# Kernel optimization log

Hardware: AMD Instinct MI355X
Metric: run time of the kernel (lower is better)

## Reference

```python
import jax, jax.numpy as jnp
import numpy as np

N, D_IN, H, D_EMB = 2048, 128, 256, 64


def setup_inputs() -> dict:
    key = jax.random.key(0)
    ks = jax.random.split(key, 8)
    x = jax.random.normal(ks[0], (N, D_IN), dtype=jnp.float32)
    adj = jnp.zeros((N, N), dtype=jnp.float32)  # only its last dim is used (eye sizing)
    s = 0.05
    W0 = jax.random.normal(ks[1], (D_IN, H), dtype=jnp.float32) * s
    b0 = jnp.zeros((H,), dtype=jnp.float32)
    W1 = jax.random.normal(ks[2], (H, D_EMB), dtype=jnp.float32) * s
    b1 = jnp.zeros((D_EMB,), dtype=jnp.float32)
    W2 = jax.random.normal(ks[3], (D_IN, D_IN), dtype=jnp.float32) * s
    b2 = jnp.zeros((D_IN,), dtype=jnp.float32)
    temp = jnp.float32(0.1)
    theta = jnp.float32(0.1)
    return {"x": x, "adj": adj, "W0": W0, "b0": b0, "W1": W1, "b1": b1,
            "W2": W2, "b2": b2, "temp": temp, "theta": theta}


def reference(x, adj, W0, b0, W1, b1, W2, b2, temp, theta):
    # layer 0 (on x) and middle layer 1 (on out_x), both with ReLU activation
    out_x = jax.nn.relu(x @ W0 + b0)            # [N, H]
    emb = jax.nn.relu(out_x @ W1 + b1)          # [N, D_EMB]
    # last layer is applied to the ORIGINAL x (per the `x = model(x)` branch)
    x_last = x @ W2 + b2                        # [N, D_IN]

    # dist[i,j] = -||emb_i - emb_j||^2, computed via the gemm expansion
    sq = jnp.sum(emb * emb, axis=1)             # [N]
    dist = -(sq[:, None] + sq[None, :] - 2.0 * (emb @ emb.T))  # [N, N]

    prob = jax.nn.sigmoid((1.0 + temp) * dist + (5.0 + theta))
    A = prob + jnp.eye(adj.shape[-1], dtype=prob.dtype)        # [N, N]

    # diag(A.sum(-1))^{-1} @ A @ x_last  ==  rowwise divide by degree
    deg = jnp.sum(A, axis=-1)                   # [N]
    out = jax.nn.relu((A @ x_last) / deg[:, None])

    # sigmoid(.) > 0 everywhere, so all N*N entries are nonzero: adj_wts is the
    # full flattened adjacency (data-independent shape, jit-safe)
    adj_wts = A.reshape(-1)
    return out, adj_wts
```

## Files before the change

kernel.cpp:

```cpp
#include <hip/hip_runtime.h>
#include <hip/hip_bf16.h>


typedef short bf16x8 __attribute__((ext_vector_type(8)));
typedef float f32x4 __attribute__((ext_vector_type(4)));

__device__ __forceinline__ unsigned short f2bf(float f) {
    unsigned u = __float_as_uint(f);
    unsigned r = u + 0x7fffu + ((u >> 16) & 1u);
    return (unsigned short)(r >> 16);
}

__global__ __launch_bounds__(512) void k1_mlp(
    const float* __restrict__ x,
    const float* __restrict__ W0, const float* __restrict__ b0,
    const float* __restrict__ W1, const float* __restrict__ b1,
    const float* __restrict__ W2, const float* __restrict__ b2,
    unsigned short* __restrict__ emb_bf,
    unsigned short* __restrict__ xlT_bf,
    float* __restrict__ sq)
{
    __shared__ float xs[8 * 132];
    __shared__ float oxs[8 * 260];
    __shared__ unsigned short xls[128 * 8];
    const int t = threadIdx.x;
    const int r0 = blockIdx.x * 8;

    if (t < 256) {
        int row = t >> 5, c4 = t & 31;
        float4 v = *(const float4*)(x + (r0 + row) * 128 + c4 * 4);
        *(float4*)(&xs[row * 132 + c4 * 4]) = v;
    }
    __syncthreads();

    {
        int c = t & 255, rg = t >> 8;
        float bb = b0[c];
        float acc[4] = {bb, bb, bb, bb};
        for (int kk = 0; kk < 32; ++kk) {
            float wa = W0[(kk * 4 + 0) * 256 + c];
            float wb = W0[(kk * 4 + 1) * 256 + c];
            float wc = W0[(kk * 4 + 2) * 256 + c];
            float wd = W0[(kk * 4 + 3) * 256 + c];
            #pragma unroll
            for (int r = 0; r < 4; ++r) {
                float4 xv = *(const float4*)(&xs[(rg * 4 + r) * 132 + kk * 4]);
                acc[r] += xv.x * wa + xv.y * wb + xv.z * wc + xv.w * wd;
            }
        }
        #pragma unroll
        for (int r = 0; r < 4; ++r) oxs[(rg * 4 + r) * 260 + c] = fmaxf(acc[r], 0.0f);
    }
    __syncthreads();

    {
        int h = t & 63, r = t >> 6;
        float acc = b1[h];
        for (int kk = 0; kk < 64; ++kk) {
            float wa = W1[(kk * 4 + 0) * 64 + h];
            float wb = W1[(kk * 4 + 1) * 64 + h];
            float wc = W1[(kk * 4 + 2) * 64 + h];
            float wd = W1[(kk * 4 + 3) * 64 + h];
            float4 xv = *(const float4*)(&oxs[r * 260 + kk * 4]);
            acc += xv.x * wa + xv.y * wb + xv.z * wc + xv.w * wd;
        }
        float e = fmaxf(acc, 0.0f);
        emb_bf[(r0 + r) * 64 + h] = f2bf(e);
        float s = e * e;
        #pragma unroll
        for (int off = 32; off; off >>= 1) s += __shfl_xor(s, off);
        if (h == 0) sq[r0 + r] = s;
    }

    {
        int c = t & 127, rg = t >> 7;
        float bb = b2[c];
        float acc[2] = {bb, bb};
        for (int kk = 0; kk < 32; ++kk) {
            float wa = W2[(kk * 4 + 0) * 128 + c];
            float wb = W2[(kk * 4 + 1) * 128 + c];
            float wc = W2[(kk * 4 + 2) * 128 + c];
            float wd = W2[(kk * 4 + 3) * 128 + c];
            #pragma unroll
            for (int r = 0; r < 2; ++r) {
                float4 xv = *(const float4*)(&xs[(rg * 2 + r) * 132 + kk * 4]);
                acc[r] += xv.x * wa + xv.y * wb + xv.z * wc + xv.w * wd;
            }
        }
        unsigned short p0 = f2bf(acc[0]), p1 = f2bf(acc[1]);
        *(unsigned int*)(&xls[c * 8 + rg * 2]) = (unsigned)p0 | ((unsigned)p1 << 16);
    }
    __syncthreads();
    if (t < 128) {
        uint4 v = *(const uint4*)(&xls[t * 8]);
        *(uint4*)(&xlT_bf[t * 2048 + r0]) = v;
    }
}

__global__ __launch_bounds__(256) void k2_adj(
    const unsigned short* __restrict__ emb_bf,
    const unsigned short* __restrict__ xlT_bf,
    const float* __restrict__ sq,
    const float* __restrict__ tempp, const float* __restrict__ thetap,
    float* __restrict__ outPart,
    float* __restrict__ degPart,
    float* __restrict__ adjw,
    int iters)
{
    constexpr int LD = 88;
    __shared__ unsigned short embI[16 * LD];
    __shared__ unsigned short embJ[64 * LD];
    __shared__ unsigned short xlT[128 * LD];
    __shared__ unsigned short Ald[16 * LD];
    __shared__ float sqJ[64];
    __shared__ float sqI[16];
    __shared__ float degS[64];

    const int t = threadIdx.x;
    const int lane = t & 63;
    const int w = t >> 6;
    const int m = lane & 15;
    const int q = lane >> 4;
    const int i0 = blockIdx.x * 16;
    const int bj = blockIdx.y;
    const int jbase = bj * (iters * 64);
    const float scale = 1.0f + tempp[0];
    const float bias = 5.0f + thetap[0];

    if (t < 128) {
        int row = t >> 3, off = t & 7;
        uint4 v = *(const uint4*)(emb_bf + (i0 + row) * 64 + off * 8);
        *(uint4*)(&embI[row * LD + off * 8]) = v;
    }
    if (t < 16) sqI[t] = sq[i0 + t];

    f32x4 accF0 = {0.f, 0.f, 0.f, 0.f};
    f32x4 accF1 = {0.f, 0.f, 0.f, 0.f};
    float dega[4] = {0.f, 0.f, 0.f, 0.f};

    for (int jt = 0; jt < iters; ++jt) {
        const int j0 = jbase + jt * 64;
        __syncthreads();
        for (int ch = t; ch < 512; ch += 256) {
            int row = ch >> 3, off = ch & 7;
            uint4 v = *(const uint4*)(emb_bf + (j0 + row) * 64 + off * 8);
            *(uint4*)(&embJ[row * LD + off * 8]) = v;
        }
        for (int ch = t; ch < 1024; ch += 256) {
            int row = ch >> 3, off = ch & 7;
            uint4 v = *(const uint4*)(xlT_bf + row * 2048 + j0 + off * 8);
            *(uint4*)(&xlT[row * LD + off * 8]) = v;
        }
        if (t < 64) sqJ[t] = sq[j0 + t];
        __syncthreads();

        bf16x8 a0 = *(const bf16x8*)(&embI[m * LD + q * 8]);
        bf16x8 a1 = *(const bf16x8*)(&embI[m * LD + 32 + q * 8]);
        int jc = w * 16 + m;
        bf16x8 b0v = *(const bf16x8*)(&embJ[jc * LD + q * 8]);
        bf16x8 b1v = *(const bf16x8*)(&embJ[jc * LD + 32 + q * 8]);
        f32x4 S = {0.f, 0.f, 0.f, 0.f};
        S = __builtin_amdgcn_mfma_f32_16x16x32_bf16(a0, b0v, S, 0, 0, 0);
        S = __builtin_amdgcn_mfma_f32_16x16x32_bf16(a1, b1v, S, 0, 0, 0);

        float csqJ = sqJ[w * 16 + m];
        int gcol = j0 + w * 16 + m;
        #pragma unroll
        for (int r = 0; r < 4; ++r) {
            int grow = i0 + q * 4 + r;
            float dist = 2.0f * S[r] - sqI[q * 4 + r] - csqJ;
            float z = scale * dist + bias;
            float p = 1.0f / (1.0f + __expf(-z));
            if (grow == gcol) p += 1.0f;
            adjw[grow * 2048 + gcol] = p;
            dega[r] += p;
            Ald[(q * 4 + r) * LD + w * 16 + m] = f2bf(p);
        }
        __syncthreads();

        bf16x8 aa0 = *(const bf16x8*)(&Ald[m * LD + q * 8]);
        bf16x8 aa1 = *(const bf16x8*)(&Ald[m * LD + 32 + q * 8]);
        int n0 = w * 32 + m;
        bf16x8 bb0 = *(const bf16x8*)(&xlT[n0 * LD + q * 8]);
        bf16x8 bb1 = *(const bf16x8*)(&xlT[n0 * LD + 32 + q * 8]);
        accF0 = __builtin_amdgcn_mfma_f32_16x16x32_bf16(aa0, bb0, accF0, 0, 0, 0);
        accF0 = __builtin_amdgcn_mfma_f32_16x16x32_bf16(aa1, bb1, accF0, 0, 0, 0);
        int n1 = w * 32 + 16 + m;
        bf16x8 cc0 = *(const bf16x8*)(&xlT[n1 * LD + q * 8]);
        bf16x8 cc1 = *(const bf16x8*)(&xlT[n1 * LD + 32 + q * 8]);
        accF1 = __builtin_amdgcn_mfma_f32_16x16x32_bf16(aa0, cc0, accF1, 0, 0, 0);
        accF1 = __builtin_amdgcn_mfma_f32_16x16x32_bf16(aa1, cc1, accF1, 0, 0, 0);
    }

    #pragma unroll
    for (int r = 0; r < 4; ++r) {
        float v = dega[r];
        v += __shfl_xor(v, 1);
        v += __shfl_xor(v, 2);
        v += __shfl_xor(v, 4);
        v += __shfl_xor(v, 8);
        if (m == 0) degS[(q * 4 + r) * 4 + w] = v;
    }
    __syncthreads();
    if (t < 16)
        degPart[bj * 2048 + i0 + t] =
            degS[t * 4] + degS[t * 4 + 1] + degS[t * 4 + 2] + degS[t * 4 + 3];

    float* op = outPart + ((size_t)bj * 2048 + i0) * 128;
    #pragma unroll
    for (int r = 0; r < 4; ++r) {
        op[(q * 4 + r) * 128 + w * 32 + m] = accF0[r];
        op[(q * 4 + r) * 128 + w * 32 + 16 + m] = accF1[r];
    }
}

__global__ __launch_bounds__(256) void k3_fin(
    const float* __restrict__ outPart, const float* __restrict__ degPart,
    float* __restrict__ out, int P)
{
    int idx = blockIdx.x * 256 + threadIdx.x;
    int i = idx >> 7, c = idx & 127;
    float s = 0.f, d = 0.f;
    for (int p = 0; p < P; ++p) {
        s += outPart[((size_t)p * 2048 + i) * 128 + c];
        d += degPart[p * 2048 + i];
    }
    out[idx] = fmaxf(s / d, 0.0f);
}

extern "C" void kernel_launch(void* const* d_in, const int* in_sizes, int n_in,
                              void* d_out, int out_size, void* d_ws, size_t ws_size,
                              hipStream_t stream) {
    const float* x     = (const float*)d_in[0];
    const float* W0    = (const float*)d_in[2];
    const float* b0    = (const float*)d_in[3];
    const float* W1    = (const float*)d_in[4];
    const float* b1    = (const float*)d_in[5];
    const float* W2    = (const float*)d_in[6];
    const float* b2    = (const float*)d_in[7];
    const float* temp  = (const float*)d_in[8];
    const float* theta = (const float*)d_in[9];

    char* ws = (char*)d_ws;
    unsigned short* emb_bf = (unsigned short*)(ws);
    unsigned short* xlT_bf = (unsigned short*)(ws + 262144);
    float* sq      = (float*)(ws + 786432);
    float* degPart = (float*)(ws + 794624);
    float* outPart = (float*)(ws + 860160);

    int P = 8;
    while (P > 1 && (size_t)860160 + (size_t)P * 1048576 > ws_size) P >>= 1;
    int iters = 2048 / (P * 64);

    float* out  = (float*)d_out;
    float* adjw = (float*)d_out + 262144;

    k1_mlp<<<256, 512, 0, stream>>>(x, W0, b0, W1, b1, W2, b2, emb_bf, xlT_bf, sq);
    k2_adj<<<dim3(128, P), 256, 0, stream>>>(emb_bf, xlT_bf, sq, temp, theta,
                                             outPart, degPart, adjw, iters);
    k3_fin<<<1024, 256, 0, stream>>>(outPart, degPart, out, P);
}
```

Before: 118.1 us.

## Split adjacency build and A@x aggregation into separate kernels via bf16 A buffer

Replaces the fused adjacency-plus-aggregation kernel and its partial-sum reduction kernel with two kernels. The first computes the sigmoid adjacency in 64x128 tiles, writes both the fp32 output and a bf16 copy of A to workspace, and accumulates degree with atomics. The second does A@x_last as a streaming MFMA GEMM with a split-K of two reduced in shared memory, then normalises. This removes the per-tile syncs and the partial-output reduction pass, at the cost of an extra 8MB write and read of the bf16 A matrix through global memory.

```diff
diff --git a/kernel.cpp b/kernel.cpp
--- a/kernel.cpp
+++ b/kernel.cpp
@@ -18,7 +18,8 @@
     const float* __restrict__ W2, const float* __restrict__ b2,
     unsigned short* __restrict__ emb_bf,
     unsigned short* __restrict__ xlT_bf,
-    float* __restrict__ sq)
+    float* __restrict__ sq,
+    float* __restrict__ deg)
 {
     __shared__ float xs[8 * 132];
     __shared__ float oxs[8 * 260];
@@ -31,6 +32,7 @@
         float4 v = *(const float4*)(x + (r0 + row) * 128 + c4 * 4);
         *(float4*)(&xs[row * 132 + c4 * 4]) = v;
     }
+    if (t < 8) deg[r0 + t] = 0.0f;
     __syncthreads();
 
     {
@@ -97,101 +99,73 @@
     }
 }
 
-__global__ __launch_bounds__(256) void k2_adj(
+__global__ __launch_bounds__(256) void k2a(
     const unsigned short* __restrict__ emb_bf,
-    const unsigned short* __restrict__ xlT_bf,
     const float* __restrict__ sq,
     const float* __restrict__ tempp, const float* __restrict__ thetap,
-    float* __restrict__ outPart,
-    float* __restrict__ degPart,
     float* __restrict__ adjw,
-    int iters)
+    unsigned short* __restrict__ A_bf,
+    float* __restrict__ deg)
 {
-    constexpr int LD = 88;
-    __shared__ unsigned short embI[16 * LD];
-    __shared__ unsigned short embJ[64 * LD];
-    __shared__ unsigned short xlT[128 * LD];
-    __shared__ unsigned short Ald[16 * LD];
-    __shared__ float sqJ[64];
-    __shared__ float sqI[16];
-    __shared__ float degS[64];
+    constexpr int LD = 72;
+    __shared__ unsigned short embI[64 * LD];
+    __shared__ unsigned short embJ[128 * LD];
+    __shared__ float sqI[64];
+    __shared__ float sqJ[128];
 
     const int t = threadIdx.x;
     const int lane = t & 63;
     const int w = t >> 6;
     const int m = lane & 15;
     const int q = lane >> 4;
-    const int i0 = blockIdx.x * 16;
-    const int bj = blockIdx.y;
-    const int jbase = bj * (iters * 64);
+    const int i0 = blockIdx.x * 64;
+    const int j0 = blockIdx.y * 128;
     const float scale = 1.0f + tempp[0];
     const float bias = 5.0f + thetap[0];
 
-    if (t < 128) {
-        int row = t >> 3, off = t & 7;
-        uint4 v = *(const uint4*)(emb_bf + (i0 + row) * 64 + off * 8);
-        *(uint4*)(&embI[row * LD + off * 8]) = v;
-    }
-    if (t < 16) sqI[t] = sq[i0 + t];
-
-    f32x4 accF0 = {0.f, 0.f, 0.f, 0.f};
-    f32x4 accF1 = {0.f, 0.f, 0.f, 0.f};
+    for (int ch = t; ch < 512; ch += 256) {
+        int row = ch >> 3, off = ch & 7;
+        *(uint4*)(&embI[row * LD + off * 8]) =
+            *(const uint4*)(emb_bf + (i0 + row) * 64 + off * 8);
+    }
+    for (int ch = t; ch < 1024; ch += 256) {
+        int row = ch >> 3, off = ch & 7;
+        *(uint4*)(&embJ[row * LD + off * 8]) =
+            *(const uint4*)(emb_bf + (j0 + row) * 64 + off * 8);
+    }
+    if (t < 64) sqI[t] = sq[i0 + t];
+    if (t >= 64 && t < 192) sqJ[t - 64] = sq[j0 + t - 64];
+    __syncthreads();
+
+    const int irow = w * 16;
+    bf16x8 a0 = *(const bf16x8*)(&embI[(irow + m) * LD + q * 8]);
+    bf16x8 a1 = *(const bf16x8*)(&embI[(irow + m) * LD + 32 + q * 8]);
     float dega[4] = {0.f, 0.f, 0.f, 0.f};
 
-    for (int jt = 0; jt < iters; ++jt) {
-        const int j0 = jbase + jt * 64;
-        __syncthreads();
-        for (int ch = t; ch < 512; ch += 256) {
-            int row = ch >> 3, off = ch & 7;
-            uint4 v = *(const uint4*)(emb_bf + (j0 + row) * 64 + off * 8);
-            *(uint4*)(&embJ[row * LD + off * 8]) = v;
-        }
-        for (int ch = t; ch < 1024; ch += 256) {
-            int row = ch >> 3, off = ch & 7;
-            uint4 v = *(const uint4*)(xlT_bf + row * 2048 + j0 + off * 8);
-            *(uint4*)(&xlT[row * LD + off * 8]) = v;
-        }
-        if (t < 64) sqJ[t] = sq[j0 + t];
-        __syncthreads();
-
-        bf16x8 a0 = *(const bf16x8*)(&embI[m * LD + q * 8]);
-        bf16x8 a1 = *(const bf16x8*)(&embI[m * LD + 32 + q * 8]);
-        int jc = w * 16 + m;
-        bf16x8 b0v = *(const bf16x8*)(&embJ[jc * LD + q * 8]);
-        bf16x8 b1v = *(const bf16x8*)(&embJ[jc * LD + 32 + q * 8]);
+    #pragma unroll
+    for (int jc = 0; jc < 8; ++jc) {
+        int jcol = jc * 16 + m;
+        bf16x8 b0 = *(const bf16x8*)(&embJ[jcol * LD + q * 8]);
+        bf16x8 b1 = *(const bf16x8*)(&embJ[jcol * LD + 32 + q * 8]);
         f32x4 S = {0.f, 0.f, 0.f, 0.f};
-        S = __builtin_amdgcn_mfma_f32_16x16x32_bf16(a0, b0v, S, 0, 0, 0);
-        S = __builtin_amdgcn_mfma_f32_16x16x32_bf16(a1, b1v, S, 0, 0, 0);
-
-        float csqJ = sqJ[w * 16 + m];
-        int gcol = j0 + w * 16 + m;
+        S = __builtin_amdgcn_mfma_f32_16x16x32_bf16(a0, b0, S, 0, 0, 0);
+        S = __builtin_amdgcn_mfma_f32_16x16x32_bf16(a1, b1, S, 0, 0, 0);
+
+        float csqJ = sqJ[jc * 16 + m];
+        int gcol = j0 + jc * 16 + m;
         #pragma unroll
         for (int r = 0; r < 4; ++r) {
-            int grow = i0 + q * 4 + r;
-            float dist = 2.0f * S[r] - sqI[q * 4 + r] - csqJ;
+            int lrow = irow + q * 4 + r;
+            int grow = i0 + lrow;
+            float dist = 2.0f * S[r] - sqI[lrow] - csqJ;
             float z = scale * dist + bias;
             float p = 1.0f / (1.0f + __expf(-z));
             if (grow == gcol) p += 1.0f;
-            adjw[grow * 2048 + gcol] = p;
+            adjw[(size_t)grow * 2048 + gcol] = p;
+            A_bf[(size_t)grow * 2048 + gcol] = f2bf(p);
             dega[r] += p;
-            Ald[(q * 4 + r) * LD + w * 16 + m] = f2bf(p);
-        }
-        __syncthreads();
-
-        bf16x8 aa0 = *(const bf16x8*)(&Ald[m * LD + q * 8]);
-        bf16x8 aa1 = *(const bf16x8*)(&Ald[m * LD + 32 + q * 8]);
-        int n0 = w * 32 + m;
-        bf16x8 bb0 = *(const bf16x8*)(&xlT[n0 * LD + q * 8]);
-        bf16x8 bb1 = *(const bf16x8*)(&xlT[n0 * LD + 32 + q * 8]);
-        accF0 = __builtin_amdgcn_mfma_f32_16x16x32_bf16(aa0, bb0, accF0, 0, 0, 0);
-        accF0 = __builtin_amdgcn_mfma_f32_16x16x32_bf16(aa1, bb1, accF0, 0, 0, 0);
-        int n1 = w * 32 + 16 + m;
-        bf16x8 cc0 = *(const bf16x8*)(&xlT[n1 * LD + q * 8]);
-        bf16x8 cc1 = *(const bf16x8*)(&xlT[n1 * LD + 32 + q * 8]);
-        accF1 = __builtin_amdgcn_mfma_f32_16x16x32_bf16(aa0, cc0, accF1, 0, 0, 0);
-        accF1 = __builtin_amdgcn_mfma_f32_16x16x32_bf16(aa1, cc1, accF1, 0, 0, 0);
-    }
-
+        }
+    }
     #pragma unroll
     for (int r = 0; r < 4; ++r) {
         float v = dega[r];
@@ -199,33 +173,51 @@
         v += __shfl_xor(v, 2);
         v += __shfl_xor(v, 4);
         v += __shfl_xor(v, 8);
-        if (m == 0) degS[(q * 4 + r) * 4 + w] = v;
-    }
-    __syncthreads();
-    if (t < 16)
-        degPart[bj * 2048 + i0 + t] =
-            degS[t * 4] + degS[t * 4 + 1] + degS[t * 4 + 2] + degS[t * 4 + 3];
-
-    float* op = outPart + ((size_t)bj * 2048 + i0) * 128;
+        if (m == 0) atomicAdd(&deg[i0 + irow + q * 4 + r], v);
+    }
+}
+
+__global__ __launch_bounds__(512) void k2b(
+    const unsigned short* __restrict__ A_bf,
+    const unsigned short* __restrict__ xlT_bf,
+    const float* __restrict__ deg,
+    float* __restrict__ out)
+{
+    __shared__ float part[2 * 16 * 128];
+    const int t = threadIdx.x;
+    const int lane = t & 63;
+    const int w = t >> 6;
+    const int m = lane & 15;
+    const int q = lane >> 4;
+    const int i0 = blockIdx.x * 16;
+    const int cg = (w & 3) * 32;
+    const int kh = w >> 2;
+
+    const unsigned short* Arow = A_bf + (size_t)(i0 + m) * 2048 + kh * 1024;
+    const unsigned short* B0 = xlT_bf + (size_t)(cg + m) * 2048 + kh * 1024;
+    const unsigned short* B1 = xlT_bf + (size_t)(cg + 16 + m) * 2048 + kh * 1024;
+
+    f32x4 acc0 = {0.f, 0.f, 0.f, 0.f};
+    f32x4 acc1 = {0.f, 0.f, 0.f, 0.f};
+    #pragma unroll 4
+    for (int kk = 0; kk < 1024; kk += 32) {
+        bf16x8 a  = *(const bf16x8*)(Arow + kk + q * 8);
+        bf16x8 b0 = *(const bf16x8*)(B0 + kk + q * 8);
+        bf16x8 b1 = *(const bf16x8*)(B1 + kk + q * 8);
+        acc0 = __builtin_amdgcn_mfma_f32_16x16x32_bf16(a, b0, acc0, 0, 0, 0);
+        acc1 = __builtin_amdgcn_mfma_f32_16x16x32_bf16(a, b1, acc1, 0, 0, 0);
+    }
     #pragma unroll
     for (int r = 0; r < 4; ++r) {
-        op[(q * 4 + r) * 128 + w * 32 + m] = accF0[r];
-        op[(q * 4 + r) * 128 + w * 32 + 16 + m] = accF1[r];
-    }
-}
-
-__global__ __launch_bounds__(256) void k3_fin(
-    const float* __restrict__ outPart, const float* __restrict__ degPart,
-    float* __restrict__ out, int P)
-{
-    int idx = blockIdx.x * 256 + threadIdx.x;
-    int i = idx >> 7, c = idx & 127;
-    float s = 0.f, d = 0.f;
-    for (int p = 0; p < P; ++p) {
-        s += outPart[((size_t)p * 2048 + i) * 128 + c];
-        d += degPart[p * 2048 + i];
-    }
-    out[idx] = fmaxf(s / d, 0.0f);
+        part[kh * 2048 + (q * 4 + r) * 128 + cg + m] = acc0[r];
+        part[kh * 2048 + (q * 4 + r) * 128 + cg + 16 + m] = acc1[r];
+    }
+    __syncthreads();
+    for (int idx = t; idx < 2048; idx += 512) {
+        int r = idx >> 7, c = idx & 127;
+        float s = part[r * 128 + c] + part[2048 + r * 128 + c];
+        out[(size_t)(i0 + r) * 128 + c] = fmaxf(s / deg[i0 + r], 0.0f);
+    }
 }
 
 extern "C" void kernel_launch(void* const* d_in, const int* in_sizes, int n_in,
@@ -244,19 +236,16 @@
     char* ws = (char*)d_ws;
     unsigned short* emb_bf = (unsigned short*)(ws);
     unsigned short* xlT_bf = (unsigned short*)(ws + 262144);
-    float* sq      = (float*)(ws + 786432);
-    float* degPart = (float*)(ws + 794624);
-    float* outPart = (float*)(ws + 860160);
-
-    int P = 8;
-    while (P > 1 && (size_t)860160 + (size_t)P * 1048576 > ws_size) P >>= 1;
-    int iters = 2048 / (P * 64);
+    float* sq   = (float*)(ws + 786432);
+    float* deg  = (float*)(ws + 794624);
+    unsigned short* A_bf = (unsigned short*)(ws + 802816);
 
     float* out  = (float*)d_out;
     float* adjw = (float*)d_out + 262144;
 
-    k1_mlp<<<256, 512, 0, stream>>>(x, W0, b0, W1, b1, W2, b2, emb_bf, xlT_bf, sq);
-    k2_adj<<<dim3(128, P), 256, 0, stream>>>(emb_bf, xlT_bf, sq, temp, theta,
-                                             outPart, degPart, adjw, iters);
-    k3_fin<<<1024, 256, 0, stream>>>(outPart, degPart, out, P);
-}
+    k1_mlp<<<256, 512, 0, stream>>>(x, W0, b0, W1, b1, W2, b2,
+                                    emb_bf, xlT_bf, sq, deg);
+    k2a<<<dim3(32, 16), 256, 0, stream>>>(emb_bf, sq, temp, theta,
+                                          adjw, A_bf, deg);
+    k2b<<<128, 512, 0, stream>>>(A_bf, xlT_bf, deg, out);
+}
```

After: 132.0 us. 11.8% more time.
